# Optimization experiments

Measured on AMD Instinct MI355X. Metric: run time of the kernel, lower is better.

## Reference

```python
import jax, jax.numpy as jnp
import numpy as np

E = 500_000
B = 64
N_INC = 64
E_INC = 64
U_INC = 64
W_INC = 2
H1 = 128   # edge_model_mlp1_hidden_sizes[0]
H2 = 128   # edge_model_mlp1_hidden_sizes[1] == GRU hidden
E_OUT = 64
DIM_IN = E_INC + 2 * N_INC + U_INC      # 256
DIM_W2 = DIM_IN // 2                     # 128
DIM_X1 = DIM_IN + DIM_W2                 # 384
LN_EPS = 1e-5


def _layernorm(x, g, b):
    mu = jnp.mean(x, axis=-1, keepdims=True)
    var = jnp.mean(jnp.square(x - mu), axis=-1, keepdims=True)
    return (x - mu) * jax.lax.rsqrt(var + LN_EPS) * g + b


def setup_inputs() -> dict:
    key = jax.random.key(0)
    ks = jax.random.split(key, 20)
    s = lambda k, shape: (jax.random.normal(k, shape, dtype=jnp.float32) * 0.05)
    return {
        "src": jax.random.normal(ks[0], (E, N_INC), dtype=jnp.float32),
        "dest": jax.random.normal(ks[1], (E, N_INC), dtype=jnp.float32),
        "edge_attr": jax.random.normal(ks[2], (E, E_INC), dtype=jnp.float32),
        "h": jax.random.normal(ks[3], (E, H2), dtype=jnp.float32),
        "u": jax.random.normal(ks[4], (B, U_INC), dtype=jnp.float32),
        "batch": jax.random.randint(ks[5], (E,), 0, B, dtype=jnp.int32),
        "winding": jax.random.uniform(ks[6], (E, W_INC), dtype=jnp.float32),
        # winding_mlp: Linear(W_INC, DIM_W2) + LayerNorm
        "Ww": s(ks[7], (DIM_W2, W_INC)),
        "bw": jnp.zeros((DIM_W2,), jnp.float32),
        "gw": jnp.ones((DIM_W2,), jnp.float32),
        "betaw": jnp.zeros((DIM_W2,), jnp.float32),
        # mlp1: Linear(DIM_X1, H1) + LayerNorm
        "W1": s(ks[8], (H1, DIM_X1)),
        "b1": jnp.zeros((H1,), jnp.float32),
        "g1": jnp.ones((H1,), jnp.float32),
        "beta1": jnp.zeros((H1,), jnp.float32),
        # GRU(H1 -> H2), 1 layer
        "Wih": s(ks[9], (3 * H2, H1)),
        "Whh": s(ks[10], (3 * H2, H2)),
        "bih": jnp.zeros((3 * H2,), jnp.float32),
        "bhh": jnp.zeros((3 * H2,), jnp.float32),
        # mlp_x: Linear(H2, E_OUT)
        "Wx": s(ks[11], (E_OUT, H2)),
        "bx": jnp.zeros((E_OUT,), jnp.float32),
    }


def reference(src, dest, edge_attr, h, u, batch, winding,
              Ww, bw, gw, betaw, W1, b1, g1, beta1,
              Wih, Whh, bih, bhh, Wx, bx):
    # winding_mlp: Linear + LayerNorm + ReLU
    w = jax.nn.relu(_layernorm(winding @ Ww.T + bw, gw, betaw))      # [E, DIM_W2]
    # concat [src, dest, edge_attr, u[batch], w]
    x = jnp.concatenate([src, dest, edge_attr, u[batch], w], axis=1)  # [E, DIM_X1]
    # mlp1: Linear + LayerNorm + ReLU
    x = jax.nn.relu(_layernorm(x @ W1.T + b1, g1, beta1))             # [E, H1]
    # single-step GRU (PyTorch gate order: r, z, n)
    gi = x @ Wih.T + bih                                              # [E, 3*H2]
    gh = h @ Whh.T + bhh                                              # [E, 3*H2]
    i_r, i_z, i_n = jnp.split(gi, 3, axis=-1)
    h_r, h_z, h_n = jnp.split(gh, 3, axis=-1)
    r = jax.nn.sigmoid(i_r + h_r)
    z = jax.nn.sigmoid(i_z + h_z)
    n = jnp.tanh(i_n + r * h_n)
    h_new = (1.0 - z) * n + z * h                                     # [E, H2]
    x_out = h_new @ Wx.T + bx                                         # [E, E_OUT]
    return (x_out, h_new)
```

## Files before the change

### kernel.cpp

```cpp
#include <hip/hip_runtime.h>
#include <hip/hip_bf16.h>

#define E_TOTAL 500000
#define NB2 7813
#define NTIL 7813
#define GBLK 512

typedef __attribute__((ext_vector_type(8))) short bf16x8;
typedef __attribute__((ext_vector_type(4))) float f32x4;

#define MFMA(a, b, c) __builtin_amdgcn_mfma_f32_16x16x32_bf16((a), (b), (c), 0, 0, 0)

typedef __attribute__((address_space(1))) const void GV;
typedef __attribute__((address_space(3))) void LV;

__device__ __forceinline__ void lbar() {
    asm volatile("s_waitcnt lgkmcnt(0)" ::: "memory");
    __builtin_amdgcn_s_barrier();
}
__device__ __forceinline__ unsigned int pack2(float x, float y) {
    unsigned int xb = __builtin_bit_cast(unsigned int, x) + 0x8000u;
    unsigned int yb = __builtin_bit_cast(unsigned int, y) + 0x8000u;
    return __builtin_amdgcn_perm(yb, xb, 0x07060302u);
}
__device__ __forceinline__ float b2f(unsigned short s) {
    return __bfloat162float(__builtin_bit_cast(__hip_bfloat16, s));
}
__device__ __forceinline__ float sigm(float x) { return 1.f / (1.f + __expf(-x)); }
__device__ __forceinline__ float tanh_fast(float x) {
    float t = __expf(-2.f * x);
    return (1.f - t) / (1.f + t);
}
__device__ __forceinline__ char* swzp(void* base, int row, int rowBytes, int colByte) {
    return (char*)base + row * rowBytes + (colByte ^ ((row & 7) << 4));
}

__global__ void wconv_kernel(const float* __restrict__ W1, const float* __restrict__ Wih,
                             const float* __restrict__ Whh, const float* __restrict__ Wx,
                             unsigned short* __restrict__ out) {
    int i = blockIdx.x * 256 + threadIdx.x;
    if (i >= 155648) return;
    float v;
    if      (i < 49152)  v = W1[i];
    else if (i < 98304)  v = Wih[i - 49152];
    else if (i < 147456) v = Whh[i - 98304];
    else                 v = Wx[i - 147456];
    unsigned int b = __builtin_bit_cast(unsigned int, v) + 0x8000u;
    out[i] = (unsigned short)(b >> 16);
}

struct SmemM {
    unsigned short x1[64][384];
    float lns[64][4];
    float ln2[64][4];
    float par[640];
};

__global__ __launch_bounds__(256) void mlp1_kernel(
    const float* __restrict__ src, const float* __restrict__ dst,
    const float* __restrict__ eat, const float* __restrict__ u,
    const int* __restrict__ batch, const float* __restrict__ winding,
    const float* __restrict__ hin,
    const float* __restrict__ Ww, const float* __restrict__ bw,
    const float* __restrict__ gw, const float* __restrict__ betaw,
    const float* __restrict__ b1, const float* __restrict__ g1,
    const float* __restrict__ beta1,
    const unsigned short* __restrict__ W1bf,
    unsigned short* __restrict__ ybf, unsigned short* __restrict__ hbf)
{
    __shared__ SmemM sm;
    const int tid  = threadIdx.x;
    const int wave = tid >> 6;
    const int lane = tid & 63;
    const int lhi  = lane >> 4;
    const int llo  = lane & 15;
    const size_t e0 = (size_t)blockIdx.x * 64;

    for (int i = tid; i < 640; i += 256) {
        float v;
        if      (i < 256) v = Ww[i];
        else if (i < 384) v = bw[i - 256];
        else if (i < 512) v = gw[i - 384];
        else              v = betaw[i - 512];
        sm.par[i] = v;
    }
    lbar();

    #pragma unroll
    for (int it = 0; it < 4; ++it) {
        int q   = it * 256 + tid;
        int row = q >> 4;
        int c4  = (q & 15) << 2;
        size_t e = e0 + row; if (e >= E_TOTAL) e = E_TOTAL - 1;
        float4 a = *(const float4*)(src + e * 64 + c4);
        float4 b = *(const float4*)(dst + e * 64 + c4);
        float4 c = *(const float4*)(eat + e * 64 + c4);
        int bi   = batch[e];
        float4 d = *(const float4*)(u + (size_t)bi * 64 + c4);
        uint2 pa = make_uint2(pack2(a.x, a.y), pack2(a.z, a.w));
        uint2 pb = make_uint2(pack2(b.x, b.y), pack2(b.z, b.w));
        uint2 pc = make_uint2(pack2(c.x, c.y), pack2(c.z, c.w));
        uint2 pd = make_uint2(pack2(d.x, d.y), pack2(d.z, d.w));
        *(uint2*)swzp(sm.x1, row, 768, 2 * c4)       = pa;
        *(uint2*)swzp(sm.x1, row, 768, 128 + 2 * c4) = pb;
        *(uint2*)swzp(sm.x1, row, 768, 256 + 2 * c4) = pc;
        *(uint2*)swzp(sm.x1, row, 768, 384 + 2 * c4) = pd;
    }
    #pragma unroll
    for (int it = 0; it < 4; ++it) {
        int q   = it * 256 + tid;
        int row = q >> 4;
        int c8  = (q & 15) << 3;
        size_t e = e0 + row;
        size_t ec = e < E_TOTAL ? e : E_TOTAL - 1;
        float4 a = *(const float4*)(hin + ec * 128 + c8);
        float4 b = *(const float4*)(hin + ec * 128 + c8 + 4);
        uint4 pk;
        pk.x = pack2(a.x, a.y); pk.y = pack2(a.z, a.w);
        pk.z = pack2(b.x, b.y); pk.w = pack2(b.z, b.w);
        if (e < E_TOTAL) *(uint4*)(hbf + e * 128 + c8) = pk;
    }
    {
        int row = tid >> 2;
        int seg = tid & 3;
        size_t e = e0 + row; if (e >= E_TOTAL) e = E_TOTAL - 1;
        float wi0 = winding[e * 2], wi1 = winding[e * 2 + 1];
        float vals[32]; float s = 0.f, s2 = 0.f;
        #pragma unroll
        for (int j = 0; j < 32; ++j) {
            int jj = seg * 32 + j;
            float v = fmaf(wi0, sm.par[2 * jj], fmaf(wi1, sm.par[2 * jj + 1], sm.par[256 + jj]));
            vals[j] = v; s += v; s2 += v * v;
        }
        s  += __shfl_xor(s, 1);  s  += __shfl_xor(s, 2);
        s2 += __shfl_xor(s2, 1); s2 += __shfl_xor(s2, 2);
        float mean = s * (1.f / 128.f);
        float var  = fmaxf(s2 * (1.f / 128.f) - mean * mean, 0.f);
        float inv  = rsqrtf(var + 1e-5f);
        #pragma unroll
        for (int j4 = 0; j4 < 8; ++j4) {
            int jj = seg * 32 + j4 * 4;
            float v0 = fmaxf((vals[j4*4+0] - mean) * inv * sm.par[384 + jj]     + sm.par[512 + jj],     0.f);
            float v1 = fmaxf((vals[j4*4+1] - mean) * inv * sm.par[384 + jj + 1] + sm.par[512 + jj + 1], 0.f);
            float v2 = fmaxf((vals[j4*4+2] - mean) * inv * sm.par[384 + jj + 2] + sm.par[512 + jj + 2], 0.f);
            float v3 = fmaxf((vals[j4*4+3] - mean) * inv * sm.par[384 + jj + 3] + sm.par[512 + jj + 3], 0.f);
            uint2 pk = make_uint2(pack2(v0, v1), pack2(v2, v3));
            *(uint2*)swzp(sm.x1, row, 768, 512 + seg * 64 + j4 * 8) = pk;
        }
    }
    lbar();

    f32x4 acc[2][4];
    #pragma unroll
    for (int nt = 0; nt < 2; ++nt)
        #pragma unroll
        for (int mt = 0; mt < 4; ++mt) acc[nt][mt] = (f32x4){0.f, 0.f, 0.f, 0.f};
    {
        const unsigned short* wp = W1bf + (size_t)(wave * 32 + llo) * 384 + lhi * 8;
        #pragma unroll
        for (int ks = 0; ks < 12; ++ks) {
            bf16x8 wf0 = *(const bf16x8*)(wp + ks * 32);
            bf16x8 wf1 = *(const bf16x8*)(wp + 16 * 384 + ks * 32);
            #pragma unroll
            for (int mt = 0; mt < 4; ++mt) {
                bf16x8 xf = *(const bf16x8*)swzp(sm.x1, mt * 16 + llo, 768, ks * 64 + lhi * 16);
                acc[0][mt] = MFMA(wf0, xf, acc[0][mt]);
                acc[1][mt] = MFMA(wf1, xf, acc[1][mt]);
            }
        }
    }
    {
        float4 b1q0 = *(const float4*)&b1[wave * 32 + lhi * 4];
        float4 b1q1 = *(const float4*)&b1[wave * 32 + 16 + lhi * 4];
        #pragma unroll
        for (int mt = 0; mt < 4; ++mt) {
            float s = 0.f, s2 = 0.f;
            #pragma unroll
            for (int r = 0; r < 4; ++r) {
                float v0 = acc[0][mt][r] + ((const float*)&b1q0)[r];
                float v1 = acc[1][mt][r] + ((const float*)&b1q1)[r];
                acc[0][mt][r] = v0; acc[1][mt][r] = v1;
                s += v0 + v1; s2 += v0 * v0 + v1 * v1;
            }
            s  += __shfl_xor(s, 16);  s  += __shfl_xor(s, 32);
            s2 += __shfl_xor(s2, 16); s2 += __shfl_xor(s2, 32);
            if (lane < 16) { sm.lns[mt * 16 + llo][wave] = s; sm.ln2[mt * 16 + llo][wave] = s2; }
        }
    }
    lbar();

    {
        float4 g1q0  = *(const float4*)&g1[wave * 32 + lhi * 4];
        float4 g1q1  = *(const float4*)&g1[wave * 32 + 16 + lhi * 4];
        float4 be1q0 = *(const float4*)&beta1[wave * 32 + lhi * 4];
        float4 be1q1 = *(const float4*)&beta1[wave * 32 + 16 + lhi * 4];
        #pragma unroll
        for (int mt = 0; mt < 4; ++mt) {
            int edge = mt * 16 + llo;
            size_t e = e0 + edge;
            float4 sa = *(const float4*)&sm.lns[edge][0];
            float4 ta = *(const float4*)&sm.ln2[edge][0];
            float s  = sa.x + sa.y + sa.z + sa.w;
            float s2 = ta.x + ta.y + ta.z + ta.w;
            float mean = s * (1.f / 128.f);
            float var  = fmaxf(s2 * (1.f / 128.f) - mean * mean, 0.f);
            float inv  = rsqrtf(var + 1e-5f);
            if (e < E_TOTAL) {
                #pragma unroll
                for (int nt = 0; nt < 2; ++nt) {
                    const float4& gq  = nt ? g1q1 : g1q0;
                    const float4& beq = nt ? be1q1 : be1q0;
                    float v0 = fmaxf((acc[nt][mt][0] - mean) * inv * gq.x + beq.x, 0.f);
                    float v1 = fmaxf((acc[nt][mt][1] - mean) * inv * gq.y + beq.y, 0.f);
                    float v2 = fmaxf((acc[nt][mt][2] - mean) * inv * gq.z + beq.z, 0.f);
                    float v3 = fmaxf((acc[nt][mt][3] - mean) * inv * gq.w + beq.w, 0.f);
                    uint2 pk = make_uint2(pack2(v0, v1), pack2(v2, v3));
                    int f = wave * 32 + nt * 16 + lhi * 4;
                    *(uint2*)(ybf + e * 128 + f) = pk;
                }
            }
        }
    }
}

__global__ __launch_bounds__(512, 2) void gru_kernel(
    const unsigned short* __restrict__ ybf, const unsigned short* hbf,
    const float* __restrict__ bih, const float* __restrict__ bhh,
    const float* __restrict__ bx,
    const unsigned short* __restrict__ Wihbf, const unsigned short* __restrict__ Whhbf,
    const unsigned short* __restrict__ Wxbf,
    float* xout, float* __restrict__ hout)
{
    __shared__ unsigned short smy[2][64][128];
    __shared__ unsigned short smh[2][64][128];
    __shared__ unsigned short smn[64][128];
    const int tid  = threadIdx.x;
    const int wave = tid >> 6;
    const int lane = tid & 63;
    const int lhi  = lane >> 4;
    const int llo  = lane & 15;
    const int f    = wave * 16 + lhi * 4;
    const int fx   = (wave & 3) * 16 + lhi * 4;
    const int eh   = (wave >> 2) * 32;

    float4 br_, bz_;
    {
        float4 a0 = *(const float4*)&bih[f],       c0 = *(const float4*)&bhh[f];
        float4 a1 = *(const float4*)&bih[128 + f], c1 = *(const float4*)&bhh[128 + f];
        br_.x = a0.x + c0.x; br_.y = a0.y + c0.y; br_.z = a0.z + c0.z; br_.w = a0.w + c0.w;
        bz_.x = a1.x + c1.x; bz_.y = a1.y + c1.y; bz_.z = a1.z + c1.z; bz_.w = a1.w + c1.w;
    }
    const float4 bi2 = *(const float4*)&bih[256 + f];
    const float4 bh2 = *(const float4*)&bhh[256 + f];
    const float4 bxq = *(const float4*)&bx[fx];
    const unsigned short* pi = Wihbf + (size_t)(wave * 16 + llo) * 128 + lhi * 8;
    const unsigned short* pw = Whhbf + (size_t)(wave * 16 + llo) * 128 + lhi * 8;
    const unsigned short* px = Wxbf + (size_t)((wave & 3) * 16 + llo) * 128 + lhi * 8;

    auto stage = [&](int t, int buf) {
        const size_t eb = (size_t)t * 64;
        #pragma unroll
        for (int j = 0; j < 2; ++j) {
            int O = j * 8192 + tid * 16;
            int row = O >> 8, colB = O & 255;
            size_t e = eb + row; if (e >= E_TOTAL) e = E_TOTAL - 1;
            unsigned lc = (unsigned)colB ^ (((unsigned)row & 7u) << 4);
            __builtin_amdgcn_global_load_lds((GV*)((const char*)ybf + e * 256 + lc),
                                             (LV*)((char*)&smy[buf][0][0] + O), 16, 0, 0);
            __builtin_amdgcn_global_load_lds((GV*)((const char*)hbf + e * 256 + lc),
                                             (LV*)((char*)&smh[buf][0][0] + O), 16, 0, 0);
        }
    };

    int cur = 0;
    stage(blockIdx.x, 0);
    asm volatile("s_waitcnt vmcnt(0)" ::: "memory");
    lbar();

    for (int t = blockIdx.x; t < NTIL; t += GBLK) {
        const size_t e0 = (size_t)t * 64;
        {
            int tn = t + GBLK; if (tn >= NTIL) tn = t;
            stage(tn, cur ^ 1);
        }

        f32x4 gr[4], gz[4], gn[4], gh[4];
        #pragma unroll
        for (int mt = 0; mt < 4; ++mt) {
            gr[mt] = (f32x4){0.f,0.f,0.f,0.f}; gz[mt] = (f32x4){0.f,0.f,0.f,0.f};
            gn[mt] = (f32x4){0.f,0.f,0.f,0.f}; gh[mt] = (f32x4){0.f,0.f,0.f,0.f};
        }
        #pragma unroll
        for (int ks = 0; ks < 4; ++ks) {
            bf16x8 wr = *(const bf16x8*)(pi + ks * 32);
            bf16x8 wz = *(const bf16x8*)(pi + 128 * 128 + ks * 32);
            bf16x8 wn = *(const bf16x8*)(pi + 256 * 128 + ks * 32);
            bf16x8 vr = *(const bf16x8*)(pw + ks * 32);
            bf16x8 vz = *(const bf16x8*)(pw + 128 * 128 + ks * 32);
            bf16x8 vn = *(const bf16x8*)(pw + 256 * 128 + ks * 32);
            #pragma unroll
            for (int mt = 0; mt < 4; ++mt) {
                int row = mt * 16 + llo;
                bf16x8 ay = *(const bf16x8*)swzp(smy[cur], row, 256, ks * 64 + lhi * 16);
                bf16x8 ah = *(const bf16x8*)swzp(smh[cur], row, 256, ks * 64 + lhi * 16);
                gr[mt] = MFMA(wr, ay, gr[mt]);  gr[mt] = MFMA(vr, ah, gr[mt]);
                gz[mt] = MFMA(wz, ay, gz[mt]);  gz[mt] = MFMA(vz, ah, gz[mt]);
                gn[mt] = MFMA(wn, ay, gn[mt]);  gh[mt] = MFMA(vn, ah, gh[mt]);
            }
        }

        #pragma unroll
        for (int mt = 0; mt < 4; ++mt) {
            int row = mt * 16 + llo;
            ushort4 hp = *(const ushort4*)swzp(smh[cur], row, 256, 2 * f);
            float4 ho;
            #pragma unroll
            for (int r = 0; r < 4; ++r) {
                float rr = sigm(gr[mt][r] + ((const float*)&br_)[r]);
                float zz = sigm(gz[mt][r] + ((const float*)&bz_)[r]);
                float nn = tanh_fast(gn[mt][r] + ((const float*)&bi2)[r]
                                     + rr * (gh[mt][r] + ((const float*)&bh2)[r]));
                float hv = b2f(((const unsigned short*)&hp)[r]);
                ((float*)&ho)[r] = (1.f - zz) * nn + zz * hv;
            }
            unsigned int p0 = pack2(ho.x, ho.y), p1 = pack2(ho.z, ho.w);
            ushort4 pk;
            pk.x = (unsigned short)(p0 & 0xffffu); pk.y = (unsigned short)(p0 >> 16);
            pk.z = (unsigned short)(p1 & 0xffffu); pk.w = (unsigned short)(p1 >> 16);
            *(ushort4*)swzp(smn, row, 256, 2 * f) = pk;
            size_t e = e0 + row;
            if (e < E_TOTAL) *(float4*)(hout + e * 128 + f) = ho;
        }
        lbar();

        {
            f32x4 a3[2];
            a3[0] = (f32x4){0.f,0.f,0.f,0.f}; a3[1] = (f32x4){0.f,0.f,0.f,0.f};
            #pragma unroll
            for (int ks = 0; ks < 4; ++ks) {
                bf16x8 wf = *(const bf16x8*)(px + ks * 32);
                #pragma unroll
                for (int mt = 0; mt < 2; ++mt) {
                    bf16x8 bh = *(const bf16x8*)swzp(smn, eh + mt * 16 + llo, 256, ks * 64 + lhi * 16);
                    a3[mt] = MFMA(wf, bh, a3[mt]);
                }
            }
            #pragma unroll
            for (int mt = 0; mt < 2; ++mt) {
                size_t e = e0 + eh + mt * 16 + llo;
                float4 o;
                o.x = a3[mt][0] + bxq.x; o.y = a3[mt][1] + bxq.y;
                o.z = a3[mt][2] + bxq.z; o.w = a3[mt][3] + bxq.w;
                if (e < E_TOTAL) *(float4*)(xout + e * 64 + fx) = o;
            }
        }

        if (e0 + 64 <= E_TOTAL) asm volatile("s_waitcnt vmcnt(6)" ::: "memory");
        else                    asm volatile("s_waitcnt vmcnt(0)" ::: "memory");
        lbar();
        cur ^= 1;
    }
}

extern "C" void kernel_launch(void* const* d_in, const int* in_sizes, int n_in,
                              void* d_out, int out_size, void* d_ws, size_t ws_size,
                              hipStream_t stream)
{
    const float* src   = (const float*)d_in[0];
    const float* dst   = (const float*)d_in[1];
    const float* eat   = (const float*)d_in[2];
    const float* hin   = (const float*)d_in[3];
    const float* u     = (const float*)d_in[4];
    const int*   bat   = (const int*)d_in[5];
    const float* wind  = (const float*)d_in[6];
    const float* Ww    = (const float*)d_in[7];
    const float* bw    = (const float*)d_in[8];
    const float* gw    = (const float*)d_in[9];
    const float* betaw = (const float*)d_in[10];
    const float* W1    = (const float*)d_in[11];
    const float* b1    = (const float*)d_in[12];
    const float* g1    = (const float*)d_in[13];
    const float* beta1 = (const float*)d_in[14];
    const float* Wih   = (const float*)d_in[15];
    const float* Whh   = (const float*)d_in[16];
    const float* bih   = (const float*)d_in[17];
    const float* bhh   = (const float*)d_in[18];
    const float* Wx    = (const float*)d_in[19];
    const float* bx    = (const float*)d_in[20];

    unsigned short* ybf  = (unsigned short*)d_ws;
    unsigned short* wbuf = ybf + 64000000ull;

    float* xout = (float*)d_out;
    float* hout = xout + (size_t)E_TOTAL * 64;
    unsigned short* hbf = (unsigned short*)d_out;

    wconv_kernel<<<608, 256, 0, stream>>>(W1, Wih, Whh, Wx, wbuf);

    mlp1_kernel<<<NB2, 256, 0, stream>>>(
        src, dst, eat, u, bat, wind, hin, Ww, bw, gw, betaw,
        b1, g1, beta1, wbuf, ybf, hbf);

    gru_kernel<<<GBLK, 512, 0, stream>>>(
        ybf, hbf, bih, bhh, bx,
        wbuf + 49152, wbuf + 98304, wbuf + 147456,
        xout, hout);
}
```

Measured before the change: 503.7 us.

## Make mlp1 persistent with register prefetch; hold GRU weights in registers

The mlp1 kernel becomes persistent with 512 blocks looping over tiles. It prefetches the next tile's src/dest/edge_attr/u/h/winding loads into registers while the current tile's MFMA and layernorm run. The GRU kernel drops to 256 persistent blocks at one block per CU and hoists all Wih/Whh/Wx bf16 fragments into registers, so weights are no longer reloaded from global every tile. This adds heavy register pressure (launch bounds set to 1 block) and lowers occupancy, relying on explicit prefetch to hide latency.

```diff
diff --git a/kernel.cpp b/kernel.cpp
--- a/kernel.cpp
+++ b/kernel.cpp
@@ -2,9 +2,9 @@
 #include <hip/hip_bf16.h>
 
 #define E_TOTAL 500000
-#define NB2 7813
+#define NB2 512
 #define NTIL 7813
-#define GBLK 512
+#define GBLK 256
 
 typedef __attribute__((ext_vector_type(8))) short bf16x8;
 typedef __attribute__((ext_vector_type(4))) float f32x4;
@@ -56,7 +56,7 @@
     float par[640];
 };
 
-__global__ __launch_bounds__(256) void mlp1_kernel(
+__global__ __launch_bounds__(256, 1) void mlp1_kernel(
     const float* __restrict__ src, const float* __restrict__ dst,
     const float* __restrict__ eat, const float* __restrict__ u,
     const int* __restrict__ batch, const float* __restrict__ winding,
@@ -74,7 +74,6 @@
     const int lane = tid & 63;
     const int lhi  = lane >> 4;
     const int llo  = lane & 15;
-    const size_t e0 = (size_t)blockIdx.x * 64;
 
     for (int i = tid; i < 640; i += 256) {
         float v;
@@ -86,144 +85,167 @@
     }
     lbar();
 
-    #pragma unroll
-    for (int it = 0; it < 4; ++it) {
-        int q   = it * 256 + tid;
-        int row = q >> 4;
-        int c4  = (q & 15) << 2;
-        size_t e = e0 + row; if (e >= E_TOTAL) e = E_TOTAL - 1;
-        float4 a = *(const float4*)(src + e * 64 + c4);
-        float4 b = *(const float4*)(dst + e * 64 + c4);
-        float4 c = *(const float4*)(eat + e * 64 + c4);
-        int bi   = batch[e];
-        float4 d = *(const float4*)(u + (size_t)bi * 64 + c4);
-        uint2 pa = make_uint2(pack2(a.x, a.y), pack2(a.z, a.w));
-        uint2 pb = make_uint2(pack2(b.x, b.y), pack2(b.z, b.w));
-        uint2 pc = make_uint2(pack2(c.x, c.y), pack2(c.z, c.w));
-        uint2 pd = make_uint2(pack2(d.x, d.y), pack2(d.z, d.w));
-        *(uint2*)swzp(sm.x1, row, 768, 2 * c4)       = pa;
-        *(uint2*)swzp(sm.x1, row, 768, 128 + 2 * c4) = pb;
-        *(uint2*)swzp(sm.x1, row, 768, 256 + 2 * c4) = pc;
-        *(uint2*)swzp(sm.x1, row, 768, 384 + 2 * c4) = pd;
-    }
-    #pragma unroll
-    for (int it = 0; it < 4; ++it) {
-        int q   = it * 256 + tid;
-        int row = q >> 4;
-        int c8  = (q & 15) << 3;
-        size_t e = e0 + row;
-        size_t ec = e < E_TOTAL ? e : E_TOTAL - 1;
-        float4 a = *(const float4*)(hin + ec * 128 + c8);
-        float4 b = *(const float4*)(hin + ec * 128 + c8 + 4);
-        uint4 pk;
-        pk.x = pack2(a.x, a.y); pk.y = pack2(a.z, a.w);
-        pk.z = pack2(b.x, b.y); pk.w = pack2(b.z, b.w);
-        if (e < E_TOTAL) *(uint4*)(hbf + e * 128 + c8) = pk;
-    }
-    {
-        int row = tid >> 2;
-        int seg = tid & 3;
-        size_t e = e0 + row; if (e >= E_TOTAL) e = E_TOTAL - 1;
-        float wi0 = winding[e * 2], wi1 = winding[e * 2 + 1];
-        float vals[32]; float s = 0.f, s2 = 0.f;
-        #pragma unroll
-        for (int j = 0; j < 32; ++j) {
-            int jj = seg * 32 + j;
-            float v = fmaf(wi0, sm.par[2 * jj], fmaf(wi1, sm.par[2 * jj + 1], sm.par[256 + jj]));
-            vals[j] = v; s += v; s2 += v * v;
-        }
-        s  += __shfl_xor(s, 1);  s  += __shfl_xor(s, 2);
-        s2 += __shfl_xor(s2, 1); s2 += __shfl_xor(s2, 2);
-        float mean = s * (1.f / 128.f);
-        float var  = fmaxf(s2 * (1.f / 128.f) - mean * mean, 0.f);
-        float inv  = rsqrtf(var + 1e-5f);
-        #pragma unroll
-        for (int j4 = 0; j4 < 8; ++j4) {
-            int jj = seg * 32 + j4 * 4;
-            float v0 = fmaxf((vals[j4*4+0] - mean) * inv * sm.par[384 + jj]     + sm.par[512 + jj],     0.f);
-            float v1 = fmaxf((vals[j4*4+1] - mean) * inv * sm.par[384 + jj + 1] + sm.par[512 + jj + 1], 0.f);
-            float v2 = fmaxf((vals[j4*4+2] - mean) * inv * sm.par[384 + jj + 2] + sm.par[512 + jj + 2], 0.f);
-            float v3 = fmaxf((vals[j4*4+3] - mean) * inv * sm.par[384 + jj + 3] + sm.par[512 + jj + 3], 0.f);
-            uint2 pk = make_uint2(pack2(v0, v1), pack2(v2, v3));
-            *(uint2*)swzp(sm.x1, row, 768, 512 + seg * 64 + j4 * 8) = pk;
-        }
-    }
-    lbar();
-
-    f32x4 acc[2][4];
-    #pragma unroll
-    for (int nt = 0; nt < 2; ++nt)
-        #pragma unroll
-        for (int mt = 0; mt < 4; ++mt) acc[nt][mt] = (f32x4){0.f, 0.f, 0.f, 0.f};
-    {
-        const unsigned short* wp = W1bf + (size_t)(wave * 32 + llo) * 384 + lhi * 8;
-        #pragma unroll
-        for (int ks = 0; ks < 12; ++ks) {
-            bf16x8 wf0 = *(const bf16x8*)(wp + ks * 32);
-            bf16x8 wf1 = *(const bf16x8*)(wp + 16 * 384 + ks * 32);
-            #pragma unroll
-            for (int mt = 0; mt < 4; ++mt) {
-                bf16x8 xf = *(const bf16x8*)swzp(sm.x1, mt * 16 + llo, 768, ks * 64 + lhi * 16);
-                acc[0][mt] = MFMA(wf0, xf, acc[0][mt]);
-                acc[1][mt] = MFMA(wf1, xf, acc[1][mt]);
-            }
-        }
-    }
-    {
-        float4 b1q0 = *(const float4*)&b1[wave * 32 + lhi * 4];
-        float4 b1q1 = *(const float4*)&b1[wave * 32 + 16 + lhi * 4];
-        #pragma unroll
-        for (int mt = 0; mt < 4; ++mt) {
-            float s = 0.f, s2 = 0.f;
-            #pragma unroll
-            for (int r = 0; r < 4; ++r) {
-                float v0 = acc[0][mt][r] + ((const float*)&b1q0)[r];
-                float v1 = acc[1][mt][r] + ((const float*)&b1q1)[r];
-                acc[0][mt][r] = v0; acc[1][mt][r] = v1;
-                s += v0 + v1; s2 += v0 * v0 + v1 * v1;
-            }
-            s  += __shfl_xor(s, 16);  s  += __shfl_xor(s, 32);
-            s2 += __shfl_xor(s2, 16); s2 += __shfl_xor(s2, 32);
-            if (lane < 16) { sm.lns[mt * 16 + llo][wave] = s; sm.ln2[mt * 16 + llo][wave] = s2; }
-        }
-    }
-    lbar();
-
-    {
-        float4 g1q0  = *(const float4*)&g1[wave * 32 + lhi * 4];
-        float4 g1q1  = *(const float4*)&g1[wave * 32 + 16 + lhi * 4];
-        float4 be1q0 = *(const float4*)&beta1[wave * 32 + lhi * 4];
-        float4 be1q1 = *(const float4*)&beta1[wave * 32 + 16 + lhi * 4];
-        #pragma unroll
-        for (int mt = 0; mt < 4; ++mt) {
-            int edge = mt * 16 + llo;
-            size_t e = e0 + edge;
-            float4 sa = *(const float4*)&sm.lns[edge][0];
-            float4 ta = *(const float4*)&sm.ln2[edge][0];
-            float s  = sa.x + sa.y + sa.z + sa.w;
-            float s2 = ta.x + ta.y + ta.z + ta.w;
+    float4 pa[4], pb[4], pc[4], pd[4], ph[4][2];
+    float w0, w1;
+    auto issue = [&](int t) {
+        const size_t eb = (size_t)t * 64;
+        #pragma unroll
+        for (int it = 0; it < 4; ++it) {
+            int q = it * 256 + tid; int row = q >> 4; int c4 = (q & 15) << 2;
+            size_t e = eb + row; if (e >= E_TOTAL) e = E_TOTAL - 1;
+            pa[it] = *(const float4*)(src + e * 64 + c4);
+            pb[it] = *(const float4*)(dst + e * 64 + c4);
+            pc[it] = *(const float4*)(eat + e * 64 + c4);
+            int bi = batch[e];
+            pd[it] = *(const float4*)(u + (size_t)bi * 64 + c4);
+        }
+        #pragma unroll
+        for (int it = 0; it < 4; ++it) {
+            int q = it * 256 + tid; int row = q >> 4; int c8 = (q & 15) << 3;
+            size_t e = eb + row; if (e >= E_TOTAL) e = E_TOTAL - 1;
+            ph[it][0] = *(const float4*)(hin + e * 128 + c8);
+            ph[it][1] = *(const float4*)(hin + e * 128 + c8 + 4);
+        }
+        {
+            int row = tid >> 2;
+            size_t e = eb + row; if (e >= E_TOTAL) e = E_TOTAL - 1;
+            w0 = winding[e * 2]; w1 = winding[e * 2 + 1];
+        }
+    };
+    issue(blockIdx.x);
+
+    for (int t = blockIdx.x; t < NTIL; t += NB2) {
+        const size_t e0 = (size_t)t * 64;
+
+        #pragma unroll
+        for (int it = 0; it < 4; ++it) {
+            int q   = it * 256 + tid;
+            int row = q >> 4;
+            int c4  = (q & 15) << 2;
+            uint2 qa = make_uint2(pack2(pa[it].x, pa[it].y), pack2(pa[it].z, pa[it].w));
+            uint2 qb = make_uint2(pack2(pb[it].x, pb[it].y), pack2(pb[it].z, pb[it].w));
+            uint2 qc = make_uint2(pack2(pc[it].x, pc[it].y), pack2(pc[it].z, pc[it].w));
+            uint2 qd = make_uint2(pack2(pd[it].x, pd[it].y), pack2(pd[it].z, pd[it].w));
+            *(uint2*)swzp(sm.x1, row, 768, 2 * c4)       = qa;
+            *(uint2*)swzp(sm.x1, row, 768, 128 + 2 * c4) = qb;
+            *(uint2*)swzp(sm.x1, row, 768, 256 + 2 * c4) = qc;
+            *(uint2*)swzp(sm.x1, row, 768, 384 + 2 * c4) = qd;
+        }
+        #pragma unroll
+        for (int it = 0; it < 4; ++it) {
+            int q   = it * 256 + tid;
+            int row = q >> 4;
+            int c8  = (q & 15) << 3;
+            size_t e = e0 + row;
+            uint4 pk;
+            pk.x = pack2(ph[it][0].x, ph[it][0].y); pk.y = pack2(ph[it][0].z, ph[it][0].w);
+            pk.z = pack2(ph[it][1].x, ph[it][1].y); pk.w = pack2(ph[it][1].z, ph[it][1].w);
+            if (e < E_TOTAL) *(uint4*)(hbf + e * 128 + c8) = pk;
+        }
+        {
+            int row = tid >> 2;
+            int seg = tid & 3;
+            float vals[32]; float s = 0.f, s2 = 0.f;
+            #pragma unroll
+            for (int j = 0; j < 32; ++j) {
+                int jj = seg * 32 + j;
+                float v = fmaf(w0, sm.par[2 * jj], fmaf(w1, sm.par[2 * jj + 1], sm.par[256 + jj]));
+                vals[j] = v; s += v; s2 += v * v;
+            }
+            s  += __shfl_xor(s, 1);  s  += __shfl_xor(s, 2);
+            s2 += __shfl_xor(s2, 1); s2 += __shfl_xor(s2, 2);
             float mean = s * (1.f / 128.f);
             float var  = fmaxf(s2 * (1.f / 128.f) - mean * mean, 0.f);
             float inv  = rsqrtf(var + 1e-5f);
-            if (e < E_TOTAL) {
+            #pragma unroll
+            for (int j4 = 0; j4 < 8; ++j4) {
+                int jj = seg * 32 + j4 * 4;
+                float v0 = fmaxf((vals[j4*4+0] - mean) * inv * sm.par[384 + jj]     + sm.par[512 + jj],     0.f);
+                float v1 = fmaxf((vals[j4*4+1] - mean) * inv * sm.par[384 + jj + 1] + sm.par[512 + jj + 1], 0.f);
+                float v2 = fmaxf((vals[j4*4+2] - mean) * inv * sm.par[384 + jj + 2] + sm.par[512 + jj + 2], 0.f);
+                float v3 = fmaxf((vals[j4*4+3] - mean) * inv * sm.par[384 + jj + 3] + sm.par[512 + jj + 3], 0.f);
+                uint2 pk = make_uint2(pack2(v0, v1), pack2(v2, v3));
+                *(uint2*)swzp(sm.x1, row, 768, 512 + seg * 64 + j4 * 8) = pk;
+            }
+        }
+        { int tn = t + NB2; issue(tn < NTIL ? tn : t); }
+        lbar();
+
+        f32x4 acc[2][4];
+        #pragma unroll
+        for (int nt = 0; nt < 2; ++nt)
+            #pragma unroll
+            for (int mt = 0; mt < 4; ++mt) acc[nt][mt] = (f32x4){0.f, 0.f, 0.f, 0.f};
+        {
+            const unsigned short* wp = W1bf + (size_t)(wave * 32 + llo) * 384 + lhi * 8;
+            #pragma unroll
+            for (int ks = 0; ks < 12; ++ks) {
+                bf16x8 wf0 = *(const bf16x8*)(wp + ks * 32);
+                bf16x8 wf1 = *(const bf16x8*)(wp + 16 * 384 + ks * 32);
                 #pragma unroll
-                for (int nt = 0; nt < 2; ++nt) {
-                    const float4& gq  = nt ? g1q1 : g1q0;
-                    const float4& beq = nt ? be1q1 : be1q0;
-                    float v0 = fmaxf((acc[nt][mt][0] - mean) * inv * gq.x + beq.x, 0.f);
-                    float v1 = fmaxf((acc[nt][mt][1] - mean) * inv * gq.y + beq.y, 0.f);
-                    float v2 = fmaxf((acc[nt][mt][2] - mean) * inv * gq.z + beq.z, 0.f);
-                    float v3 = fmaxf((acc[nt][mt][3] - mean) * inv * gq.w + beq.w, 0.f);
-                    uint2 pk = make_uint2(pack2(v0, v1), pack2(v2, v3));
-                    int f = wave * 32 + nt * 16 + lhi * 4;
-                    *(uint2*)(ybf + e * 128 + f) = pk;
+                for (int mt = 0; mt < 4; ++mt) {
+                    bf16x8 xf = *(const bf16x8*)swzp(sm.x1, mt * 16 + llo, 768, ks * 64 + lhi * 16);
+                    acc[0][mt] = MFMA(wf0, xf, acc[0][mt]);
+                    acc[1][mt] = MFMA(wf1, xf, acc[1][mt]);
                 }
             }
         }
+        {
+            float4 b1q0 = *(const float4*)&b1[wave * 32 + lhi * 4];
+            float4 b1q1 = *(const float4*)&b1[wave * 32 + 16 + lhi * 4];
+            #pragma unroll
+            for (int mt = 0; mt < 4; ++mt) {
+                float s = 0.f, s2 = 0.f;
+                #pragma unroll
+                for (int r = 0; r < 4; ++r) {
+                    float v0 = acc[0][mt][r] + ((const float*)&b1q0)[r];
+                    float v1 = acc[1][mt][r] + ((const float*)&b1q1)[r];
+                    acc[0][mt][r] = v0; acc[1][mt][r] = v1;
+                    s += v0 + v1; s2 += v0 * v0 + v1 * v1;
+                }
+                s  += __shfl_xor(s, 16);  s  += __shfl_xor(s, 32);
+                s2 += __shfl_xor(s2, 16); s2 += __shfl_xor(s2, 32);
+                if (lane < 16) { sm.lns[mt * 16 + llo][wave] = s; sm.ln2[mt * 16 + llo][wave] = s2; }
+            }
+        }
+        lbar();
+
+        {
+            float4 g1q0  = *(const float4*)&g1[wave * 32 + lhi * 4];
+            float4 g1q1  = *(const float4*)&g1[wave * 32 + 16 + lhi * 4];
+            float4 be1q0 = *(const float4*)&beta1[wave * 32 + lhi * 4];
+            float4 be1q1 = *(const float4*)&beta1[wave * 32 + 16 + lhi * 4];
+            #pragma unroll
+            for (int mt = 0; mt < 4; ++mt) {
+                int edge = mt * 16 + llo;
+                size_t e = e0 + edge;
+                float4 sa = *(const float4*)&sm.lns[edge][0];
+                float4 ta = *(const float4*)&sm.ln2[edge][0];
+                float s  = sa.x + sa.y + sa.z + sa.w;
+                float s2 = ta.x + ta.y + ta.z + ta.w;
+                float mean = s * (1.f / 128.f);
+                float var  = fmaxf(s2 * (1.f / 128.f) - mean * mean, 0.f);
+                float inv  = rsqrtf(var + 1e-5f);
+                if (e < E_TOTAL) {
+                    #pragma unroll
+                    for (int nt = 0; nt < 2; ++nt) {
+                        const float4& gq  = nt ? g1q1 : g1q0;
+                        const float4& beq = nt ? be1q1 : be1q0;
+                        float v0 = fmaxf((acc[nt][mt][0] - mean) * inv * gq.x + beq.x, 0.f);
+                        float v1 = fmaxf((acc[nt][mt][1] - mean) * inv * gq.y + beq.y, 0.f);
+                        float v2 = fmaxf((acc[nt][mt][2] - mean) * inv * gq.z + beq.z, 0.f);
+                        float v3 = fmaxf((acc[nt][mt][3] - mean) * inv * gq.w + beq.w, 0.f);
+                        uint2 pk = make_uint2(pack2(v0, v1), pack2(v2, v3));
+                        int f = wave * 32 + nt * 16 + lhi * 4;
+                        *(uint2*)(ybf + e * 128 + f) = pk;
+                    }
+                }
+            }
+        }
     }
 }
 
-__global__ __launch_bounds__(512, 2) void gru_kernel(
+__global__ __launch_bounds__(512, 1) void gru_kernel(
     const unsigned short* __restrict__ ybf, const unsigned short* hbf,
     const float* __restrict__ bih, const float* __restrict__ bhh,
     const float* __restrict__ bx,
@@ -253,9 +275,23 @@
     const float4 bi2 = *(const float4*)&bih[256 + f];
     const float4 bh2 = *(const float4*)&bhh[256 + f];
     const float4 bxq = *(const float4*)&bx[fx];
-    const unsigned short* pi = Wihbf + (size_t)(wave * 16 + llo) * 128 + lhi * 8;
-    const unsigned short* pw = Whhbf + (size_t)(wave * 16 + llo) * 128 + lhi * 8;
-    const unsigned short* px = Wxbf + (size_t)((wave & 3) * 16 + llo) * 128 + lhi * 8;
+
+    bf16x8 Wr[4], Wz[4], Wn[4], Vr[4], Vz[4], Vn[4], Px[4];
+    {
+        const unsigned short* pi = Wihbf + (size_t)(wave * 16 + llo) * 128 + lhi * 8;
+        const unsigned short* pw = Whhbf + (size_t)(wave * 16 + llo) * 128 + lhi * 8;
+        const unsigned short* px = Wxbf + (size_t)((wave & 3) * 16 + llo) * 128 + lhi * 8;
+        #pragma unroll
+        for (int ks = 0; ks < 4; ++ks) {
+            Wr[ks] = *(const bf16x8*)(pi + ks * 32);
+            Wz[ks] = *(const bf16x8*)(pi + 128 * 128 + ks * 32);
+            Wn[ks] = *(const bf16x8*)(pi + 256 * 128 + ks * 32);
+            Vr[ks] = *(const bf16x8*)(pw + ks * 32);
+            Vz[ks] = *(const bf16x8*)(pw + 128 * 128 + ks * 32);
+            Vn[ks] = *(const bf16x8*)(pw + 256 * 128 + ks * 32);
+            Px[ks] = *(const bf16x8*)(px + ks * 32);
+        }
+    }
 
     auto stage = [&](int t, int buf) {
         const size_t eb = (size_t)t * 64;
@@ -292,20 +328,14 @@
         }
         #pragma unroll
         for (int ks = 0; ks < 4; ++ks) {
-            bf16x8 wr = *(const bf16x8*)(pi + ks * 32);
-            bf16x8 wz = *(const bf16x8*)(pi + 128 * 128 + ks * 32);
-            bf16x8 wn = *(const bf16x8*)(pi + 256 * 128 + ks * 32);
-            bf16x8 vr = *(const bf16x8*)(pw + ks * 32);
-            bf16x8 vz = *(const bf16x8*)(pw + 128 * 128 + ks * 32);
-            bf16x8 vn = *(const bf16x8*)(pw + 256 * 128 + ks * 32);
             #pragma unroll
             for (int mt = 0; mt < 4; ++mt) {
                 int row = mt * 16 + llo;
                 bf16x8 ay = *(const bf16x8*)swzp(smy[cur], row, 256, ks * 64 + lhi * 16);
                 bf16x8 ah = *(const bf16x8*)swzp(smh[cur], row, 256, ks * 64 + lhi * 16);
-                gr[mt] = MFMA(wr, ay, gr[mt]);  gr[mt] = MFMA(vr, ah, gr[mt]);
-                gz[mt] = MFMA(wz, ay, gz[mt]);  gz[mt] = MFMA(vz, ah, gz[mt]);
-                gn[mt] = MFMA(wn, ay, gn[mt]);  gh[mt] = MFMA(vn, ah, gh[mt]);
+                gr[mt] = MFMA(Wr[ks], ay, gr[mt]);  gr[mt] = MFMA(Vr[ks], ah, gr[mt]);
+                gz[mt] = MFMA(Wz[ks], ay, gz[mt]);  gz[mt] = MFMA(Vz[ks], ah, gz[mt]);
+                gn[mt] = MFMA(Wn[ks], ay, gn[mt]);  gh[mt] = MFMA(Vn[ks], ah, gh[mt]);
             }
         }
 
@@ -338,11 +368,10 @@
             a3[0] = (f32x4){0.f,0.f,0.f,0.f}; a3[1] = (f32x4){0.f,0.f,0.f,0.f};
             #pragma unroll
             for (int ks = 0; ks < 4; ++ks) {
-                bf16x8 wf = *(const bf16x8*)(px + ks * 32);
                 #pragma unroll
                 for (int mt = 0; mt < 2; ++mt) {
                     bf16x8 bh = *(const bf16x8*)swzp(smn, eh + mt * 16 + llo, 256, ks * 64 + lhi * 16);
-                    a3[mt] = MFMA(wf, bh, a3[mt]);
+                    a3[mt] = MFMA(Px[ks], bh, a3[mt]);
                 }
             }
             #pragma unroll
```

Result: slower. 628.5 us (+24.8%).
